# Optimization experiments

Measured on AMD Instinct MI355X. Metric: run time of the kernel, lower is better.

The kernel has to match this reference:

```python
import jax, jax.numpy as jnp
import numpy as np

N, L, S, H, E, D = 4, 1024, 1024, 16, 64, 64

def setup_inputs() -> dict:
    key = jax.random.key(0)
    kq, kk, kv = jax.random.split(key, 3)
    return {
        "queries": jax.random.normal(kq, (N, L, H, E), dtype=jnp.float32),
        "keys": jax.random.normal(kk, (N, S, H, E), dtype=jnp.float32),
        "values": jax.random.normal(kv, (N, S, H, D), dtype=jnp.float32),
        "attn_mask_add": jnp.zeros((L, S), dtype=jnp.float32),
        "key_lengths_add": jnp.zeros((N, S), dtype=jnp.float32),
    }

def reference(queries, keys, values, attn_mask_add, key_lengths_add):
    E_dim = queries.shape[-1]
    softmax_temp = 1.0 / jnp.sqrt(jnp.float32(E_dim))
    # scores: [N, H, L, S]
    QK = jnp.einsum('nlhe,nshe->nhls', queries, keys)
    QK = QK + attn_mask_add[None, None, :, :]
    QK = QK + key_lengths_add[:, None, None, :]
    A = jax.nn.softmax(softmax_temp * QK, axis=-1)  # dropout disabled (p=0)
    V = jnp.einsum('nhls,nshd->nlhd', A, values)
    return V
```

## Files before the change

kernel.cpp:

```cpp
#include <hip/hip_runtime.h>

typedef _Float16 f16x8  __attribute__((ext_vector_type(8)));
typedef _Float16 f16x4  __attribute__((ext_vector_type(4)));
typedef __fp16   hf2    __attribute__((ext_vector_type(2)));
typedef float    f32x4  __attribute__((ext_vector_type(4)));
typedef float    f32x16 __attribute__((ext_vector_type(16)));

namespace {
constexpr int kN = 4, kL = 1024, kS = 1024, kH = 16, kE = 64, kD = 64;
constexpr int kRowF = kH * kE;
constexpr int KVB = 64;
constexpr int NCH = kS / KVB;
constexpr float SCL = 0.125f * 1.44269504088896340736f;
}

__device__ __forceinline__ unsigned pku(float a, float b) {
  union { hf2 h; unsigned u; } u;
  u.h = __builtin_amdgcn_cvt_pkrtz(a, b);
  return u.u;
}
__device__ __forceinline__ f16x4 pk4(float a, float b, float c, float d) {
  union { hf2 h2[2]; f16x4 v; } u;
  u.h2[0] = __builtin_amdgcn_cvt_pkrtz(a, b);
  u.h2[1] = __builtin_amdgcn_cvt_pkrtz(c, d);
  return u.v;
}
__device__ __forceinline__ float xmax32(float t) {
  union { float f; unsigned u; } tu; tu.f = t;
  auto P = __builtin_amdgcn_permlane32_swap(tu.u, tu.u, false, false);
  union { unsigned u; float f; } a, b; a.u = P[0]; b.u = P[1];
  return fmaxf(a.f, b.f);
}
__device__ __forceinline__ float xsum32(float t) {
  union { float f; unsigned u; } tu; tu.f = t;
  auto P = __builtin_amdgcn_permlane32_swap(tu.u, tu.u, false, false);
  union { unsigned u; float f; } a, b; a.u = P[0]; b.u = P[1];
  return a.f + b.f;
}

__global__ __launch_bounds__(256)
void flag_kernel(const float* __restrict__ M, const float* __restrict__ KLN,
                 unsigned* __restrict__ F)
{
  constexpr size_t nM = (size_t)kL * kS / 4, nK = (size_t)kN * kS / 4;
  unsigned any = 0;
  for (size_t i = (size_t)blockIdx.x * 256 + threadIdx.x; i < nM + nK;
       i += (size_t)gridDim.x * 256) {
    const f32x4 v = (i < nM) ? reinterpret_cast<const f32x4*>(M)[i]
                             : reinterpret_cast<const f32x4*>(KLN)[i - nM];
    #pragma unroll
    for (int r = 0; r < 4; ++r)
      any |= (__float_as_uint(v[r]) << 1);
  }
  if (__any(any != 0) && (threadIdx.x & 63) == 0) atomicOr(F, 1u);
}

__global__ __launch_bounds__(512, 1)
void attn_fwd_kernel(const float* __restrict__ Q, const float* __restrict__ K,
                     const float* __restrict__ V, const float* __restrict__ M,
                     const float* __restrict__ KLN, float* __restrict__ O,
                     const unsigned* __restrict__ F)
{
  __shared__ _Float16 Ks[2][KVB * 64];
  __shared__ _Float16 Vt[2][kD * 64];

  const int tid  = threadIdx.x;
  const int lane = tid & 63;
  const int wave = tid >> 6;
  const int l31  = lane & 31;
  const int hi   = lane >> 5;
  const bool kRole = (wave < 4);
  const int srow = (tid >> 4) & 15;
  const int scol = tid & 15;

  const int useMask = F ? (int)F[0] : 1;

  const int swz = ((blockIdx.x & 7) << 5) | (blockIdx.x >> 3);
  const int nh = swz >> 2, qb = swz & 3;
  const int h = nh & (kH - 1), n = nh >> 4;
  const int qrow = qb * 256 + wave * 32 + l31;

  const float* Kp = K + ((size_t)n * kS * kH + h) * kE;
  const float* Vp = V + ((size_t)n * kS * kH + h) * kD;
  const float* Lp = KLN + (size_t)n * kS;
  const float* Mp = M + (size_t)qrow * kS;

  f16x8 qf[4];
  {
    const float* Qp = Q + ((size_t)((size_t)n * kL + qrow) * kH + h) * kE;
    #pragma unroll
    for (int ec = 0; ec < 4; ++ec) {
      const f32x4 a = *reinterpret_cast<const f32x4*>(Qp + 16*ec + 8*hi);
      const f32x4 b = *reinterpret_cast<const f32x4*>(Qp + 16*ec + 8*hi + 4);
      union { f16x4 h4[2]; f16x8 v; } u;
      u.h4[0] = pk4(a[0]*SCL, a[1]*SCL, a[2]*SCL, a[3]*SCL);
      u.h4[1] = pk4(b[0]*SCL, b[1]*SCL, b[2]*SCL, b[3]*SCL);
      qf[ec] = u.v;
    }
  }

  const int kxor = (l31 & 7) << 1;
  const int d0 = l31,      d1 = 32 + l31;
  const int keyv0 = ((4*((d0>>2)&3) + (d0&3)) ^ (d0>>2)) & 15;
  const int keyv1 = ((4*((d1>>2)&3) + (d1&3)) ^ (d1>>2)) & 15;
  const int vrowb0 = d0 * 64, vrowb1 = d1 * 64;
  int hwv[4];
  #pragma unroll
  for (int jd = 0; jd < 4; ++jd)
    hwv[jd] = ((4*(scol & 3) + jd) ^ scol) & 15;

  const f32x16 z16 = {0,0,0,0, 0,0,0,0, 0,0,0,0, 0,0,0,0};
  f32x16 aA0 = z16, aA1 = z16, aB0 = z16, aB1 = z16;
  float mA = -1e30f, lA = 0.f, mB = -1e30f, lB = 0.f;

  f32x4 sg[4];
  auto load_kv = [&](int sbase) {
    if (kRole) {
      #pragma unroll
      for (int i = 0; i < 4; ++i)
        sg[i] = *reinterpret_cast<const f32x4*>(Kp + (size_t)(sbase + 16*i + srow) * kRowF + 4*scol);
    } else {
      #pragma unroll
      for (int js = 0; js < 4; ++js)
        sg[js] = *reinterpret_cast<const f32x4*>(Vp + (size_t)(sbase + 4*srow + js) * kRowF + 4*scol);
    }
  };
  auto kv_write = [&](int buf) {
    if (kRole) {
      #pragma unroll
      for (int i = 0; i < 4; ++i) {
        const int s = 16*i + srow;
        *reinterpret_cast<f16x4*>(&Ks[buf][s*64 + ((scol ^ ((s & 7) << 1)) << 2)]) =
            pk4(sg[i][0], sg[i][1], sg[i][2], sg[i][3]);
      }
    } else {
      #pragma unroll
      for (int jd = 0; jd < 4; ++jd) {
        const int d = 4*scol + jd;
        *reinterpret_cast<f16x4*>(&Vt[buf][d*64 + ((srow ^ hwv[jd]) << 2)]) =
            pk4(sg[0][jd], sg[1][jd], sg[2][jd], sg[3][jd]);
      }
    }
  };

  auto half_tail = [&](const f32x16& cc, int hf, int s0h, float& mrun,
                       float& lsum, f32x16& a0, f32x16& a1) {
    float x[16];
    if (useMask) {
      #pragma unroll
      for (int m = 0; m < 4; ++m) {
        const f32x4 mv = *reinterpret_cast<const f32x4*>(Mp + s0h + 8*m + 4*hi);
        const f32x4 lv = *reinterpret_cast<const f32x4*>(Lp + s0h + 8*m + 4*hi);
        #pragma unroll
        for (int r = 0; r < 4; ++r)
          x[4*m+r] = fmaf(mv[r] + lv[r], SCL, cc[4*m+r]);
      }
    } else {
      #pragma unroll
      for (int r = 0; r < 16; ++r) x[r] = cc[r];
    }
    float mx[8];
    #pragma unroll
    for (int i = 0; i < 8; ++i) mx[i] = fmaxf(x[i], x[i+8]);
    #pragma unroll
    for (int w = 4; w >= 1; w >>= 1)
      #pragma unroll
      for (int i = 0; i < w; ++i) mx[i] = fmaxf(mx[i], mx[i+w]);
    const float tmax = xmax32(mx[0]);

    if (!__all(tmax <= mrun + 8.f)) {
      const float mnew = fmaxf(mrun, tmax);
      const float rs = __builtin_amdgcn_exp2f(mrun - mnew);
      mrun = mnew; lsum *= rs;
      a0 *= rs; a1 *= rs;
    }
    #pragma unroll
    for (int i = 0; i < 16; ++i)
      x[i] = __builtin_amdgcn_exp2f(x[i] - mrun);
    float s8[8];
    #pragma unroll
    for (int i = 0; i < 8; ++i) s8[i] = x[i] + x[i+8];
    #pragma unroll
    for (int w = 4; w >= 1; w >>= 1)
      #pragma unroll
      for (int i = 0; i < w; ++i) s8[i] += s8[i+w];
    lsum += s8[0];

    f16x8 pf0, pf1;
    {
      const unsigned k0 = pku(x[0], x[1]);
      const unsigned k1 = pku(x[2], x[3]);
      const unsigned w0 = pku(x[4], x[5]);
      const unsigned w1 = pku(x[6], x[7]);
      auto X = __builtin_amdgcn_permlane32_swap(k0, w0, false, false);
      auto Y = __builtin_amdgcn_permlane32_swap(k1, w1, false, false);
      union { unsigned u[4]; f16x8 v; } pu;
      pu.u[0] = X[0]; pu.u[1] = Y[0]; pu.u[2] = X[1]; pu.u[3] = Y[1];
      pf0 = pu.v;
    }
    {
      const unsigned k0 = pku(x[8],  x[9]);
      const unsigned k1 = pku(x[10], x[11]);
      const unsigned w0 = pku(x[12], x[13]);
      const unsigned w1 = pku(x[14], x[15]);
      auto X = __builtin_amdgcn_permlane32_swap(k0, w0, false, false);
      auto Y = __builtin_amdgcn_permlane32_swap(k1, w1, false, false);
      union { unsigned u[4]; f16x8 v; } pu;
      pu.u[0] = X[0]; pu.u[1] = Y[0]; pu.u[2] = X[1]; pu.u[3] = Y[1];
      pf1 = pu.v;
    }
    const int cur = (s0h >> 6) & 1;
    __builtin_amdgcn_s_setprio(1);
    #pragma unroll
    for (int sc = 0; sc < 2; ++sc) {
      const f16x8 pf = (sc == 0) ? pf0 : pf1;
      const int scg = hf*2 + sc;
      {
        const int sl0 = ((scg << 2) + (hi << 1)) ^ keyv0;
        union { f16x4 h4[2]; f16x8 v; } vu;
        vu.h4[0] = *reinterpret_cast<const f16x4*>(&Vt[cur][vrowb0 + (sl0 << 2)]);
        vu.h4[1] = *reinterpret_cast<const f16x4*>(&Vt[cur][vrowb0 + ((sl0 ^ 1) << 2)]);
        a0 = __builtin_amdgcn_mfma_f32_32x32x16_f16(vu.v, pf, a0, 0, 0, 0);
      }
      {
        const int sl1 = ((scg << 2) + (hi << 1)) ^ keyv1;
        union { f16x4 h4[2]; f16x8 v; } vu;
        vu.h4[0] = *reinterpret_cast<const f16x4*>(&Vt[cur][vrowb1 + (sl1 << 2)]);
        vu.h4[1] = *reinterpret_cast<const f16x4*>(&Vt[cur][vrowb1 + ((sl1 ^ 1) << 2)]);
        a1 = __builtin_amdgcn_mfma_f32_32x32x16_f16(vu.v, pf, a1, 0, 0, 0);
      }
    }
    __builtin_amdgcn_s_setprio(0);
  };

  load_kv(0);
  kv_write(0);
  load_kv(KVB);

  for (int c = 0; c < NCH; ++c) {
    const int cur = c & 1;
    const int s0 = c * KVB;
    __syncthreads();
    if (c + 1 < NCH) kv_write(cur ^ 1);
    if (c + 2 < NCH) load_kv((c + 2) * KVB);

    f32x16 ccA = z16, ccB = z16;
    __builtin_amdgcn_s_setprio(1);
    #pragma unroll
    for (int ec = 0; ec < 4; ++ec) {
      const f16x8 kfA = *reinterpret_cast<const f16x8*>(
          &Ks[cur][l31*64 + ((((ec << 2) + (hi << 1)) ^ kxor) << 2)]);
      ccA = __builtin_amdgcn_mfma_f32_32x32x16_f16(kfA, qf[ec], ccA, 0, 0, 0);
    }
    #pragma unroll
    for (int ec = 0; ec < 4; ++ec) {
      const f16x8 kfB = *reinterpret_cast<const f16x8*>(
          &Ks[cur][l31*64 + 2048 + ((((ec << 2) + (hi << 1)) ^ kxor) << 2)]);
      ccB = __builtin_amdgcn_mfma_f32_32x32x16_f16(kfB, qf[ec], ccB, 0, 0, 0);
    }
    __builtin_amdgcn_s_setprio(0);

    half_tail(ccA, 0, s0,      mA, lA, aA0, aA1);
    half_tail(ccB, 1, s0 + 32, mB, lB, aB0, aB1);
  }

  lA = xsum32(lA);
  lB = xsum32(lB);
  const float mM = fmaxf(mA, mB);
  const float wA = __builtin_amdgcn_exp2f(mA - mM);
  const float wB = __builtin_amdgcn_exp2f(mB - mM);
  const float inv = 1.f / (lA * wA + lB * wB);
  float* Op = O + (((size_t)n * kL + qrow) * kH + h) * kD;
  #pragma unroll
  for (int m = 0; m < 4; ++m) {
    f32x4 o;
    #pragma unroll
    for (int r = 0; r < 4; ++r)
      o[r] = (aA0[4*m+r] * wA + aB0[4*m+r] * wB) * inv;
    *reinterpret_cast<f32x4*>(Op + 8*m + 4*hi) = o;
  }
  #pragma unroll
  for (int m = 0; m < 4; ++m) {
    f32x4 o;
    #pragma unroll
    for (int r = 0; r < 4; ++r)
      o[r] = (aA1[4*m+r] * wA + aB1[4*m+r] * wB) * inv;
    *reinterpret_cast<f32x4*>(Op + 32 + 8*m + 4*hi) = o;
  }
}

extern "C" void kernel_launch(void* const* d_in, const int* in_sizes, int n_in,
                              void* d_out, int out_size, void* d_ws, size_t ws_size,
                              hipStream_t stream) {
  const float* Q   = (const float*)d_in[0];
  const float* K   = (const float*)d_in[1];
  const float* V   = (const float*)d_in[2];
  const float* M   = (const float*)d_in[3];
  const float* KLN = (const float*)d_in[4];
  float* O = (float*)d_out;

  unsigned* F = nullptr;
  if (ws_size >= sizeof(unsigned)) {
    F = (unsigned*)d_ws;
    hipMemsetAsync(F, 0, sizeof(unsigned), stream);
    flag_kernel<<<dim3(1024), dim3(256), 0, stream>>>(M, KLN, F);
  }

  dim3 grid(kN * kH * (kL / 256));
  dim3 block(512);
  attn_fwd_kernel<<<grid, block, 0, stream>>>(Q, K, V, M, KLN, O, F);
}
```

Measured before the change: 46.92 us.

## Process two KV chunks per barrier with a four-buffer LDS pipeline

Grows the LDS K/V staging from two to four buffers and loads and writes two 64-key chunks per iteration, so each __syncthreads covers 128 keys. The aim is to halve the number of block-wide barriers and give global prefetches more time to land. In exchange, LDS use doubles and each thread holds twice as many prefetch registers (eight f32x4), which raises register pressure.

New measurement: 47.28 us. Within noise of the previous version (+0.8%).

```diff
diff --git a/kernel.cpp b/kernel.cpp
--- a/kernel.cpp
+++ b/kernel.cpp
@@ -10,7 +10,7 @@
 constexpr int kN = 4, kL = 1024, kS = 1024, kH = 16, kE = 64, kD = 64;
 constexpr int kRowF = kH * kE;
 constexpr int KVB = 64;
-constexpr int NCH = kS / KVB;
+constexpr int NSB = kS / KVB / 2;
 constexpr float SCL = 0.125f * 1.44269504088896340736f;
 }
 
@@ -61,8 +61,8 @@
                      const float* __restrict__ KLN, float* __restrict__ O,
                      const unsigned* __restrict__ F)
 {
-  __shared__ _Float16 Ks[2][KVB * 64];
-  __shared__ _Float16 Vt[2][kD * 64];
+  __shared__ _Float16 Ks[4][KVB * 64];
+  __shared__ _Float16 Vt[4][kD * 64];
 
   const int tid  = threadIdx.x;
   const int lane = tid & 63;
@@ -113,38 +113,38 @@
   f32x16 aA0 = z16, aA1 = z16, aB0 = z16, aB1 = z16;
   float mA = -1e30f, lA = 0.f, mB = -1e30f, lB = 0.f;
 
-  f32x4 sg[4];
-  auto load_kv = [&](int sbase) {
+  f32x4 sg[8];
+  auto load_one = [&](int sbase, int off) {
     if (kRole) {
       #pragma unroll
       for (int i = 0; i < 4; ++i)
-        sg[i] = *reinterpret_cast<const f32x4*>(Kp + (size_t)(sbase + 16*i + srow) * kRowF + 4*scol);
+        sg[off+i] = *reinterpret_cast<const f32x4*>(Kp + (size_t)(sbase + 16*i + srow) * kRowF + 4*scol);
     } else {
       #pragma unroll
       for (int js = 0; js < 4; ++js)
-        sg[js] = *reinterpret_cast<const f32x4*>(Vp + (size_t)(sbase + 4*srow + js) * kRowF + 4*scol);
+        sg[off+js] = *reinterpret_cast<const f32x4*>(Vp + (size_t)(sbase + 4*srow + js) * kRowF + 4*scol);
     }
   };
-  auto kv_write = [&](int buf) {
+  auto write_one = [&](int buf, int off) {
     if (kRole) {
       #pragma unroll
       for (int i = 0; i < 4; ++i) {
         const int s = 16*i + srow;
         *reinterpret_cast<f16x4*>(&Ks[buf][s*64 + ((scol ^ ((s & 7) << 1)) << 2)]) =
-            pk4(sg[i][0], sg[i][1], sg[i][2], sg[i][3]);
+            pk4(sg[off+i][0], sg[off+i][1], sg[off+i][2], sg[off+i][3]);
       }
     } else {
       #pragma unroll
       for (int jd = 0; jd < 4; ++jd) {
         const int d = 4*scol + jd;
         *reinterpret_cast<f16x4*>(&Vt[buf][d*64 + ((srow ^ hwv[jd]) << 2)]) =
-            pk4(sg[0][jd], sg[1][jd], sg[2][jd], sg[3][jd]);
+            pk4(sg[off+0][jd], sg[off+1][jd], sg[off+2][jd], sg[off+3][jd]);
       }
     }
   };
 
-  auto half_tail = [&](const f32x16& cc, int hf, int s0h, float& mrun,
-                       float& lsum, f32x16& a0, f32x16& a1) {
+  auto half_tail = [&](const f32x16& cc, int hf, int s0h, int vbuf,
+                       float& mrun, float& lsum, f32x16& a0, f32x16& a1) {
     float x[16];
     if (useMask) {
       #pragma unroll
@@ -209,7 +209,6 @@
       pu.u[0] = X[0]; pu.u[1] = Y[0]; pu.u[2] = X[1]; pu.u[3] = Y[1];
       pf1 = pu.v;
     }
-    const int cur = (s0h >> 6) & 1;
     __builtin_amdgcn_s_setprio(1);
     #pragma unroll
     for (int sc = 0; sc < 2; ++sc) {
@@ -218,50 +217,57 @@
       {
         const int sl0 = ((scg << 2) + (hi << 1)) ^ keyv0;
         union { f16x4 h4[2]; f16x8 v; } vu;
-        vu.h4[0] = *reinterpret_cast<const f16x4*>(&Vt[cur][vrowb0 + (sl0 << 2)]);
-        vu.h4[1] = *reinterpret_cast<const f16x4*>(&Vt[cur][vrowb0 + ((sl0 ^ 1) << 2)]);
+        vu.h4[0] = *reinterpret_cast<const f16x4*>(&Vt[vbuf][vrowb0 + (sl0 << 2)]);
+        vu.h4[1] = *reinterpret_cast<const f16x4*>(&Vt[vbuf][vrowb0 + ((sl0 ^ 1) << 2)]);
         a0 = __builtin_amdgcn_mfma_f32_32x32x16_f16(vu.v, pf, a0, 0, 0, 0);
       }
       {
         const int sl1 = ((scg << 2) + (hi << 1)) ^ keyv1;
         union { f16x4 h4[2]; f16x8 v; } vu;
-        vu.h4[0] = *reinterpret_cast<const f16x4*>(&Vt[cur][vrowb1 + (sl1 << 2)]);
-        vu.h4[1] = *reinterpret_cast<const f16x4*>(&Vt[cur][vrowb1 + ((sl1 ^ 1) << 2)]);
+        vu.h4[0] = *reinterpret_cast<const f16x4*>(&Vt[vbuf][vrowb1 + (sl1 << 2)]);
+        vu.h4[1] = *reinterpret_cast<const f16x4*>(&Vt[vbuf][vrowb1 + ((sl1 ^ 1) << 2)]);
         a1 = __builtin_amdgcn_mfma_f32_32x32x16_f16(vu.v, pf, a1, 0, 0, 0);
       }
     }
     __builtin_amdgcn_s_setprio(0);
   };
 
-  load_kv(0);
-  kv_write(0);
-  load_kv(KVB);
-
-  for (int c = 0; c < NCH; ++c) {
-    const int cur = c & 1;
-    const int s0 = c * KVB;
-    __syncthreads();
-    if (c + 1 < NCH) kv_write(cur ^ 1);
-    if (c + 2 < NCH) load_kv((c + 2) * KVB);
-
+  auto do_chunk = [&](int buf, int s0) {
     f32x16 ccA = z16, ccB = z16;
     __builtin_amdgcn_s_setprio(1);
     #pragma unroll
     for (int ec = 0; ec < 4; ++ec) {
       const f16x8 kfA = *reinterpret_cast<const f16x8*>(
-          &Ks[cur][l31*64 + ((((ec << 2) + (hi << 1)) ^ kxor) << 2)]);
+          &Ks[buf][l31*64 + ((((ec << 2) + (hi << 1)) ^ kxor) << 2)]);
       ccA = __builtin_amdgcn_mfma_f32_32x32x16_f16(kfA, qf[ec], ccA, 0, 0, 0);
     }
     #pragma unroll
     for (int ec = 0; ec < 4; ++ec) {
       const f16x8 kfB = *reinterpret_cast<const f16x8*>(
-          &Ks[cur][l31*64 + 2048 + ((((ec << 2) + (hi << 1)) ^ kxor) << 2)]);
+          &Ks[buf][l31*64 + 2048 + ((((ec << 2) + (hi << 1)) ^ kxor) << 2)]);
       ccB = __builtin_amdgcn_mfma_f32_32x32x16_f16(kfB, qf[ec], ccB, 0, 0, 0);
     }
     __builtin_amdgcn_s_setprio(0);
-
-    half_tail(ccA, 0, s0,      mA, lA, aA0, aA1);
-    half_tail(ccB, 1, s0 + 32, mB, lB, aB0, aB1);
+    half_tail(ccA, 0, s0,      buf, mA, lA, aA0, aA1);
+    half_tail(ccB, 1, s0 + 32, buf, mB, lB, aB0, aB1);
+  };
+
+  load_one(0, 0);        load_one(KVB, 4);
+  write_one(0, 0);       write_one(1, 4);
+  load_one(2*KVB, 0);    load_one(3*KVB, 4);
+
+  for (int b = 0; b < NSB; ++b) {
+    __syncthreads();
+    if (b + 1 < NSB) {
+      write_one((2*b + 2) & 3, 0);
+      write_one((2*b + 3) & 3, 4);
+    }
+    if (b + 2 < NSB) {
+      load_one((2*b + 4) * KVB, 0);
+      load_one((2*b + 5) * KVB, 4);
+    }
+    do_chunk((2*b) & 3,     (2*b) * KVB);
+    do_chunk((2*b + 1) & 3, (2*b + 1) * KVB);
   }
 
   lA = xsum32(lA);
```

## Split each KV chunk across wave pairs and combine partial softmax via LDS

Applied to the files above, without the earlier changes.

Each pair of waves now shares a 32-row query tile, with each wave handling one 32-key half of every KV chunk instead of one wave doing both halves. Blocks cover 128 query rows, so the grid doubles, and the launch-bounds occupancy hint rises from 1 to 4 blocks. At the end the two halves' running max, sum and accumulators are merged through shared memory. The aim is more parallelism and shorter per-wave serial chains, in exchange for twice the K/V global loads per query row and an extra LDS reduction step.

Result: slower. 65.98 us (+40.6%).

```diff
diff --git a/kernel.cpp b/kernel.cpp
--- a/kernel.cpp
+++ b/kernel.cpp
@@ -55,30 +55,34 @@
   if (__any(any != 0) && (threadIdx.x & 63) == 0) atomicOr(F, 1u);
 }
 
-__global__ __launch_bounds__(512, 1)
+__global__ __launch_bounds__(512, 4)
 void attn_fwd_kernel(const float* __restrict__ Q, const float* __restrict__ K,
                      const float* __restrict__ V, const float* __restrict__ M,
                      const float* __restrict__ KLN, float* __restrict__ O,
                      const unsigned* __restrict__ F)
 {
-  __shared__ _Float16 Ks[2][KVB * 64];
-  __shared__ _Float16 Vt[2][kD * 64];
+  __shared__ __align__(16) char smem[35840];
+  _Float16* Ks = reinterpret_cast<_Float16*>(smem);
+  _Float16* Vt = reinterpret_cast<_Float16*>(smem + 16384);
 
   const int tid  = threadIdx.x;
   const int lane = tid & 63;
   const int wave = tid >> 6;
   const int l31  = lane & 31;
   const int hi   = lane >> 5;
+  const int qt   = wave >> 1;
+  const int half = wave & 1;
   const bool kRole = (wave < 4);
-  const int srow = (tid >> 4) & 15;
-  const int scol = tid & 15;
+  const int stid = tid & 255;
+  const int srow = stid >> 4;
+  const int scol = stid & 15;
 
   const int useMask = F ? (int)F[0] : 1;
 
-  const int swz = ((blockIdx.x & 7) << 5) | (blockIdx.x >> 3);
-  const int nh = swz >> 2, qb = swz & 3;
+  const int swz = ((blockIdx.x & 7) << 6) | (blockIdx.x >> 3);
+  const int nh = swz >> 3, qb = swz & 7;
   const int h = nh & (kH - 1), n = nh >> 4;
-  const int qrow = qb * 256 + wave * 32 + l31;
+  const int qrow = qb * 128 + qt * 32 + l31;
 
   const float* Kp = K + ((size_t)n * kS * kH + h) * kE;
   const float* Vp = V + ((size_t)n * kS * kH + h) * kD;
@@ -100,7 +104,7 @@
   }
 
   const int kxor = (l31 & 7) << 1;
-  const int d0 = l31,      d1 = 32 + l31;
+  const int d0 = l31, d1 = 32 + l31;
   const int keyv0 = ((4*((d0>>2)&3) + (d0&3)) ^ (d0>>2)) & 15;
   const int keyv1 = ((4*((d1>>2)&3) + (d1&3)) ^ (d1>>2)) & 15;
   const int vrowb0 = d0 * 64, vrowb1 = d1 * 64;
@@ -110,8 +114,8 @@
     hwv[jd] = ((4*(scol & 3) + jd) ^ scol) & 15;
 
   const f32x16 z16 = {0,0,0,0, 0,0,0,0, 0,0,0,0, 0,0,0,0};
-  f32x16 aA0 = z16, aA1 = z16, aB0 = z16, aB1 = z16;
-  float mA = -1e30f, lA = 0.f, mB = -1e30f, lB = 0.f;
+  f32x16 a0 = z16, a1 = z16;
+  float mrun = -1e30f, lsum = 0.f;
 
   f32x4 sg[4];
   auto load_kv = [&](int sbase) {
@@ -130,21 +134,40 @@
       #pragma unroll
       for (int i = 0; i < 4; ++i) {
         const int s = 16*i + srow;
-        *reinterpret_cast<f16x4*>(&Ks[buf][s*64 + ((scol ^ ((s & 7) << 1)) << 2)]) =
+        *reinterpret_cast<f16x4*>(&Ks[buf*4096 + s*64 + ((scol ^ ((s & 7) << 1)) << 2)]) =
             pk4(sg[i][0], sg[i][1], sg[i][2], sg[i][3]);
       }
     } else {
       #pragma unroll
       for (int jd = 0; jd < 4; ++jd) {
         const int d = 4*scol + jd;
-        *reinterpret_cast<f16x4*>(&Vt[buf][d*64 + ((srow ^ hwv[jd]) << 2)]) =
+        *reinterpret_cast<f16x4*>(&Vt[buf*4096 + d*64 + ((srow ^ hwv[jd]) << 2)]) =
             pk4(sg[0][jd], sg[1][jd], sg[2][jd], sg[3][jd]);
       }
     }
   };
 
-  auto half_tail = [&](const f32x16& cc, int hf, int s0h, float& mrun,
-                       float& lsum, f32x16& a0, f32x16& a1) {
+  load_kv(0);
+  kv_write(0);
+  load_kv(KVB);
+
+  for (int c = 0; c < NCH; ++c) {
+    const int cur = c & 1;
+    const int s0h = c * KVB + half * 32;
+    __syncthreads();
+    if (c + 1 < NCH) kv_write(cur ^ 1);
+    if (c + 2 < NCH) load_kv((c + 2) * KVB);
+
+    f32x16 cc = z16;
+    __builtin_amdgcn_s_setprio(1);
+    #pragma unroll
+    for (int ec = 0; ec < 4; ++ec) {
+      const f16x8 kf = *reinterpret_cast<const f16x8*>(
+          &Ks[cur*4096 + l31*64 + half*2048 + ((((ec << 2) + (hi << 1)) ^ kxor) << 2)]);
+      cc = __builtin_amdgcn_mfma_f32_32x32x16_f16(kf, qf[ec], cc, 0, 0, 0);
+    }
+    __builtin_amdgcn_s_setprio(0);
+
     float x[16];
     if (useMask) {
       #pragma unroll
@@ -159,6 +182,7 @@
       #pragma unroll
       for (int r = 0; r < 16; ++r) x[r] = cc[r];
     }
+
     float mx[8];
     #pragma unroll
     for (int i = 0; i < 8; ++i) mx[i] = fmaxf(x[i], x[i+8]);
@@ -209,83 +233,82 @@
       pu.u[0] = X[0]; pu.u[1] = Y[0]; pu.u[2] = X[1]; pu.u[3] = Y[1];
       pf1 = pu.v;
     }
-    const int cur = (s0h >> 6) & 1;
+
     __builtin_amdgcn_s_setprio(1);
     #pragma unroll
     for (int sc = 0; sc < 2; ++sc) {
       const f16x8 pf = (sc == 0) ? pf0 : pf1;
-      const int scg = hf*2 + sc;
+      const int scg = half*2 + sc;
       {
-        const int sl0 = ((scg << 2) + (hi << 1)) ^ keyv0;
+        const int sl = ((scg << 2) + (hi << 1)) ^ keyv0;
         union { f16x4 h4[2]; f16x8 v; } vu;
-        vu.h4[0] = *reinterpret_cast<const f16x4*>(&Vt[cur][vrowb0 + (sl0 << 2)]);
-        vu.h4[1] = *reinterpret_cast<const f16x4*>(&Vt[cur][vrowb0 + ((sl0 ^ 1) << 2)]);
+        vu.h4[0] = *reinterpret_cast<const f16x4*>(&Vt[cur*4096 + vrowb0 + (sl << 2)]);
+        vu.h4[1] = *reinterpret_cast<const f16x4*>(&Vt[cur*4096 + vrowb0 + ((sl ^ 1) << 2)]);
         a0 = __builtin_amdgcn_mfma_f32_32x32x16_f16(vu.v, pf, a0, 0, 0, 0);
       }
       {
-        const int sl1 = ((scg << 2) + (hi << 1)) ^ keyv1;
+        const int sl = ((scg << 2) + (hi << 1)) ^ keyv1;
         union { f16x4 h4[2]; f16x8 v; } vu;
-        vu.h4[0] = *reinterpret_cast<const f16x4*>(&Vt[cur][vrowb1 + (sl1 << 2)]);
-        vu.h4[1] = *reinterpret_cast<const f16x4*>(&Vt[cur][vrowb1 + ((sl1 ^ 1) << 2)]);
+        vu.h4[0] = *reinterpret_cast<const f16x4*>(&Vt[cur*4096 + vrowb1 + (sl << 2)]);
+        vu.h4[1] = *reinterpret_cast<const f16x4*>(&Vt[cur*4096 + vrowb1 + ((sl ^ 1) << 2)]);
         a1 = __builtin_amdgcn_mfma_f32_32x32x16_f16(vu.v, pf, a1, 0, 0, 0);
       }
     }
     __builtin_amdgcn_s_setprio(0);
-  };
-
-  load_kv(0);
-  kv_write(0);
-  load_kv(KVB);
-
-  for (int c = 0; c < NCH; ++c) {
-    const int cur = c & 1;
-    const int s0 = c * KVB;
-    __syncthreads();
-    if (c + 1 < NCH) kv_write(cur ^ 1);
-    if (c + 2 < NCH) load_kv((c + 2) * KVB);
-
-    f32x16 ccA = z16, ccB = z16;
-    __builtin_amdgcn_s_setprio(1);
-    #pragma unroll
-    for (int ec = 0; ec < 4; ++ec) {
-      const f16x8 kfA = *reinterpret_cast<const f16x8*>(
-          &Ks[cur][l31*64 + ((((ec << 2) + (hi << 1)) ^ kxor) << 2)]);
-      ccA = __builtin_amdgcn_mfma_f32_32x32x16_f16(kfA, qf[ec], ccA, 0, 0, 0);
-    }
-    #pragma unroll
-    for (int ec = 0; ec < 4; ++ec) {
-      const f16x8 kfB = *reinterpret_cast<const f16x8*>(
-          &Ks[cur][l31*64 + 2048 + ((((ec << 2) + (hi << 1)) ^ kxor) << 2)]);
-      ccB = __builtin_amdgcn_mfma_f32_32x32x16_f16(kfB, qf[ec], ccB, 0, 0, 0);
-    }
-    __builtin_amdgcn_s_setprio(0);
-
-    half_tail(ccA, 0, s0,      mA, lA, aA0, aA1);
-    half_tail(ccB, 1, s0 + 32, mB, lB, aB0, aB1);
-  }
-
-  lA = xsum32(lA);
-  lB = xsum32(lB);
-  const float mM = fmaxf(mA, mB);
-  const float wA = __builtin_amdgcn_exp2f(mA - mM);
-  const float wB = __builtin_amdgcn_exp2f(mB - mM);
-  const float inv = 1.f / (lA * wA + lB * wB);
-  float* Op = O + (((size_t)n * kL + qrow) * kH + h) * kD;
-  #pragma unroll
-  for (int m = 0; m < 4; ++m) {
-    f32x4 o;
-    #pragma unroll
-    for (int r = 0; r < 4; ++r)
-      o[r] = (aA0[4*m+r] * wA + aB0[4*m+r] * wB) * inv;
-    *reinterpret_cast<f32x4*>(Op + 8*m + 4*hi) = o;
-  }
-  #pragma unroll
-  for (int m = 0; m < 4; ++m) {
-    f32x4 o;
-    #pragma unroll
-    for (int r = 0; r < 4; ++r)
-      o[r] = (aA1[4*m+r] * wA + aB1[4*m+r] * wB) * inv;
-    *reinterpret_cast<f32x4*>(Op + 32 + 8*m + 4*hi) = o;
+  }
+
+  lsum = xsum32(lsum);
+  __syncthreads();
+  float* comb = reinterpret_cast<float*>(smem);
+  float* mlb  = reinterpret_cast<float*>(smem + 34816);
+
+  if (half == 1) {
+    #pragma unroll
+    for (int m = 0; m < 4; ++m) {
+      f32x4 o;
+      o[0] = a0[4*m+0]; o[1] = a0[4*m+1]; o[2] = a0[4*m+2]; o[3] = a0[4*m+3];
+      *reinterpret_cast<f32x4*>(&comb[qt*2176 + l31*68 + 8*m + 4*hi]) = o;
+    }
+    #pragma unroll
+    for (int m = 0; m < 4; ++m) {
+      f32x4 o;
+      o[0] = a1[4*m+0]; o[1] = a1[4*m+1]; o[2] = a1[4*m+2]; o[3] = a1[4*m+3];
+      *reinterpret_cast<f32x4*>(&comb[qt*2176 + l31*68 + 32 + 8*m + 4*hi]) = o;
+    }
+    if (hi == 0) {
+      mlb[qt*64 + l31*2 + 0] = mrun;
+      mlb[qt*64 + l31*2 + 1] = lsum;
+    }
+  }
+  __syncthreads();
+  if (half == 0) {
+    const float mB = mlb[qt*64 + l31*2 + 0];
+    const float lB = mlb[qt*64 + l31*2 + 1];
+    const float mM = fmaxf(mrun, mB);
+    const float wA = __builtin_amdgcn_exp2f(mrun - mM);
+    const float wB = __builtin_amdgcn_exp2f(mB - mM);
+    const float inv = 1.f / (lsum * wA + lB * wB);
+    float* Op = O + (((size_t)n * kL + qrow) * kH + h) * kD;
+    #pragma unroll
+    for (int m = 0; m < 4; ++m) {
+      const f32x4 pB = *reinterpret_cast<const f32x4*>(
+          &comb[qt*2176 + l31*68 + 8*m + 4*hi]);
+      f32x4 o;
+      #pragma unroll
+      for (int r = 0; r < 4; ++r)
+        o[r] = (a0[4*m+r] * wA + pB[r] * wB) * inv;
+      *reinterpret_cast<f32x4*>(Op + 8*m + 4*hi) = o;
+    }
+    #pragma unroll
+    for (int m = 0; m < 4; ++m) {
+      const f32x4 pB = *reinterpret_cast<const f32x4*>(
+          &comb[qt*2176 + l31*68 + 32 + 8*m + 4*hi]);
+      f32x4 o;
+      #pragma unroll
+      for (int r = 0; r < 4; ++r)
+        o[r] = (a1[4*m+r] * wA + pB[r] * wB) * inv;
+      *reinterpret_cast<f32x4*>(Op + 32 + 8*m + 4*hi) = o;
+    }
   }
 }
 
@@ -306,7 +329,7 @@
     flag_kernel<<<dim3(1024), dim3(256), 0, stream>>>(M, KLN, F);
   }
 
-  dim3 grid(kN * kH * (kL / 256));
+  dim3 grid(kN * kH * (kL / 128));
   dim3 block(512);
   attn_fwd_kernel<<<grid, block, 0, stream>>>(Q, K, V, M, KLN, O, F);
 }
```
